# Optimization experiments

Measured on AMD Instinct MI355X. Metric: run time of the kernel, lower is better.

## Reference

```python
import jax, jax.numpy as jnp
import numpy as np

B, S, F = 16, 1024, 768
GRID_SIZE = 5
SPLINE_ORDER = 3
GRID_MIN, GRID_MAX = -1.5, 1.5
EPS = 1e-8  # denominator guard, as in the source


def setup_inputs() -> dict:
    key = jax.random.key(0)
    kx, kc = jax.random.split(key)
    x = jax.random.normal(kx, (B, S, F), dtype=jnp.float32)
    # learned knots: per-feature copy of linspace(grid_range, grid_size)
    knots = jnp.tile(jnp.linspace(GRID_MIN, GRID_MAX, GRID_SIZE, dtype=jnp.float32), (F, 1))  # (F, G)
    coeffs = jax.random.normal(kc, (F, GRID_SIZE + SPLINE_ORDER - 1), dtype=jnp.float32)       # (F, G+k-1)
    scaler = jnp.ones((F,), dtype=jnp.float32)
    return {"x": x, "knots": knots, "coeffs": coeffs, "scaler": scaler}


def _extend_knots(knots, order):
    # pad `order` uniformly-spaced knots on each side: (F, G) -> (F, G + 2*order)
    step = (knots[:, -1] - knots[:, 0]) / (knots.shape[1] - 1)          # (F,)
    left = knots[:, :1] - step[:, None] * jnp.arange(order, 0, -1, dtype=knots.dtype)
    right = knots[:, -1:] + step[:, None] * jnp.arange(1, order + 1, dtype=knots.dtype)
    return jnp.concatenate([left, knots, right], axis=1)


def _bspline_basis(x2d, t_ext, order):
    # x2d: (N, F); t_ext: (F, K). Cox-de Boor, vectorized over basis index.
    t = t_ext[None]          # (1, F, K)
    xe = x2d[..., None]      # (N, F, 1)
    # degree 0: indicator of knot interval -> (N, F, K-1)
    b = ((xe >= t[..., :-1]) & (xe < t[..., 1:])).astype(x2d.dtype)
    for d in range(1, order + 1):
        left = (xe - t[..., :-(d + 1)]) / (t[..., d:-1] - t[..., :-(d + 1)] + EPS) * b[..., :-1]
        right = (t[..., d + 1:] - xe) / (t[..., d + 1:] - t[..., 1:-d] + EPS) * b[..., 1:]
        b = left + right
    return b                 # (N, F, K-1-order)


def reference(x, knots, coeffs, scaler):
    Bsz, Ssz, Feat = x.shape
    x2d = x.reshape(-1, Feat)                       # (N, F)
    t = _extend_knots(knots, SPLINE_ORDER)          # (F, G + 2k)
    basis = _bspline_basis(x2d, t, SPLINE_ORDER)    # (N, F, G+k-1)
    out = jnp.einsum('nfj,fj->nf', basis, coeffs) * scaler
    return out.reshape(Bsz, Ssz, Feat)
```

## Files before the change

### kernel.cpp

```cpp
#include <hip/hip_runtime.h>


constexpr int FEAT  = 768;
constexpr int GSZ   = 5;
constexpr int NCOEF = 7;
constexpr int TPF   = 13;
constexpr int BLK   = 256;
constexpr int NBLK  = 1536;

__global__ __launch_bounds__(256)
void kan_uniform(const float* __restrict__ xg,
                 const float* __restrict__ knots,
                 const float* __restrict__ coeffs,
                 const float* __restrict__ scaler,
                 float* __restrict__ outg,
                 long n2)
{
    __shared__ float clds[2 * TPF * BLK];

    const int  t  = threadIdx.x;
    const long e0 = (long)blockIdx.x * BLK + t;
    const int  f0 = (int)((2 * e0) % FEAT);

    float invh[2], nt0h[2];
#pragma unroll
    for (int c = 0; c < 2; ++c) {
        const int   f  = f0 + c;
        const float k0 = knots[f * GSZ];
        const float k4 = knots[f * GSZ + GSZ - 1];
        const float h  = (k4 - k0) * 0.25f;
        const float iv = 1.0f / h;
        invh[c] = iv;
        nt0h[c] = 3.0f - k0 * iv;
        const float sc = scaler[f];
#pragma unroll
        for (int j = 0; j < 3; ++j) {
            clds[(c * TPF + j) * BLK + t]      = 0.0f;
            clds[(c * TPF + 10 + j) * BLK + t] = 0.0f;
        }
#pragma unroll
        for (int j = 0; j < NCOEF; ++j)
            clds[(c * TPF + 3 + j) * BLK + t] = coeffs[f * NCOEF + j] * sc;
    }
    __syncthreads();

    auto eval = [&](float x, int c) -> float {
        const float g  = fmaf(x, invh[c], nt0h[c]);
        const float fi = floorf(g);
        const int   i  = (int)fi;
        const float w  = g - fi;
        const bool  inr = ((unsigned)i < 10u);
        const int   ic  = min(max(i, 0), 9);
        const float o  = 1.0f - w;
        const float w2 = w * w,  w3 = w2 * w;
        const float o2 = o * o,  o3 = o2 * o;
        const float W0 = o3 * (1.0f / 6.0f);
        const float W3 = w3 * (1.0f / 6.0f);
        const float W1 = fmaf(0.5f, w3, 2.0f / 3.0f) - w2;
        const float W2 = fmaf(0.5f, o3, 2.0f / 3.0f) - o2;
        const float* p = &clds[(c * TPF + ic) * BLK + t];
        float acc =      W0 * p[0];
        acc = fmaf(W1, p[BLK],     acc);
        acc = fmaf(W2, p[2 * BLK], acc);
        acc = fmaf(W3, p[3 * BLK], acc);
        return inr ? acc : 0.0f;
    };

    const float2* __restrict__ xp = (const float2*)xg;
    float2*       __restrict__ op = (float2*)outg;
    const long stride = (long)NBLK * BLK;

    long e = e0;
    for (; e + 3 * stride < n2; e += 4 * stride) {
        const float2 v0 = xp[e];
        const float2 v1 = xp[e + stride];
        const float2 v2 = xp[e + 2 * stride];
        const float2 v3 = xp[e + 3 * stride];
        float2 r0, r1, r2, r3;
        r0.x = eval(v0.x, 0); r0.y = eval(v0.y, 1);
        r1.x = eval(v1.x, 0); r1.y = eval(v1.y, 1);
        r2.x = eval(v2.x, 0); r2.y = eval(v2.y, 1);
        r3.x = eval(v3.x, 0); r3.y = eval(v3.y, 1);
        op[e]              = r0;
        op[e + stride]     = r1;
        op[e + 2 * stride] = r2;
        op[e + 3 * stride] = r3;
    }
    for (; e < n2; e += stride) {
        const float2 v = xp[e];
        float2 r;
        r.x = eval(v.x, 0);
        r.y = eval(v.y, 1);
        op[e] = r;
    }
}

extern "C" void kernel_launch(void* const* d_in, const int* in_sizes, int n_in,
                              void* d_out, int out_size, void* d_ws, size_t ws_size,
                              hipStream_t stream) {
    const float* x      = (const float*)d_in[0];
    const float* knots  = (const float*)d_in[1];
    const float* coeffs = (const float*)d_in[2];
    const float* scaler = (const float*)d_in[3];
    float* out = (float*)d_out;

    const long n2 = (long)in_sizes[0] / 2;

    kan_uniform<<<dim3(NBLK), dim3(BLK), 0, stream>>>(
        x, knots, coeffs, scaler, out, n2);
}
```

Before: 110.9 us.

## Precompute per-feature params in workspace and widen main loop to float4

Adds a small precompute kernel that writes inverse knot spacing, offset, and scaled coefficients to the workspace in a feature-major layout. The main kernel loads these with float4 reads, handles four features per thread with 128-bit loads and stores of x and out, and halves the grid. This cuts the per-block setup and the number of memory instructions. In exchange it adds a second launch and needs twice the LDS per block, which can reduce occupancy.

```diff
diff --git a/kernel.cpp b/kernel.cpp
--- a/kernel.cpp
+++ b/kernel.cpp
@@ -6,42 +6,61 @@
 constexpr int NCOEF = 7;
 constexpr int TPF   = 13;
 constexpr int BLK   = 256;
-constexpr int NBLK  = 1536;
+constexpr int NBLK  = 768;
 
 __global__ __launch_bounds__(256)
-void kan_uniform(const float* __restrict__ xg,
-                 const float* __restrict__ knots,
-                 const float* __restrict__ coeffs,
-                 const float* __restrict__ scaler,
-                 float* __restrict__ outg,
-                 long n2)
+void kan_precompute(const float* __restrict__ knots,
+                    const float* __restrict__ coeffs,
+                    const float* __restrict__ scaler,
+                    float* __restrict__ ws)
 {
-    __shared__ float clds[2 * TPF * BLK];
+    const int f = blockIdx.x * blockDim.x + threadIdx.x;
+    if (f >= FEAT) return;
+    const float k0 = knots[f * GSZ];
+    const float k4 = knots[f * GSZ + GSZ - 1];
+    const float h  = (k4 - k0) * 0.25f;
+    const float iv = 1.0f / h;
+    ws[0 * FEAT + f] = iv;
+    ws[1 * FEAT + f] = 3.0f - k0 * iv;
+    const float sc = scaler[f];
+#pragma unroll
+    for (int j = 0; j < NCOEF; ++j)
+        ws[(2 + j) * FEAT + f] = coeffs[f * NCOEF + j] * sc;
+}
+
+__global__ __launch_bounds__(256)
+void kan_main(const float* __restrict__ xg,
+              const float* __restrict__ ws,
+              float* __restrict__ outg,
+              long n4)
+{
+    __shared__ float clds[4 * TPF * BLK];
 
     const int  t  = threadIdx.x;
     const long e0 = (long)blockIdx.x * BLK + t;
-    const int  f0 = (int)((2 * e0) % FEAT);
+    const int  f0 = (int)((4 * e0) % FEAT);
+    const int  fq = f0 >> 2;
 
-    float invh[2], nt0h[2];
+    const float4* __restrict__ wsv = (const float4*)ws;
+    const float4 ivv = wsv[0 * (FEAT / 4) + fq];
+    const float4 ntv = wsv[1 * (FEAT / 4) + fq];
+    const float invh[4] = {ivv.x, ivv.y, ivv.z, ivv.w};
+    const float nt0h[4] = {ntv.x, ntv.y, ntv.z, ntv.w};
 #pragma unroll
-    for (int c = 0; c < 2; ++c) {
-        const int   f  = f0 + c;
-        const float k0 = knots[f * GSZ];
-        const float k4 = knots[f * GSZ + GSZ - 1];
-        const float h  = (k4 - k0) * 0.25f;
-        const float iv = 1.0f / h;
-        invh[c] = iv;
-        nt0h[c] = 3.0f - k0 * iv;
-        const float sc = scaler[f];
+    for (int j = 0; j < NCOEF; ++j) {
+        const float4 cv = wsv[(2 + j) * (FEAT / 4) + fq];
+        clds[(0 * TPF + 3 + j) * BLK + t] = cv.x;
+        clds[(1 * TPF + 3 + j) * BLK + t] = cv.y;
+        clds[(2 * TPF + 3 + j) * BLK + t] = cv.z;
+        clds[(3 * TPF + 3 + j) * BLK + t] = cv.w;
+    }
+#pragma unroll
+    for (int c = 0; c < 4; ++c)
 #pragma unroll
         for (int j = 0; j < 3; ++j) {
-            clds[(c * TPF + j) * BLK + t]      = 0.0f;
+            clds[(c * TPF + j)      * BLK + t] = 0.0f;
             clds[(c * TPF + 10 + j) * BLK + t] = 0.0f;
         }
-#pragma unroll
-        for (int j = 0; j < NCOEF; ++j)
-            clds[(c * TPF + 3 + j) * BLK + t] = coeffs[f * NCOEF + j] * sc;
-    }
     __syncthreads();
 
     auto eval = [&](float x, int c) -> float {
@@ -66,31 +85,35 @@
         return inr ? acc : 0.0f;
     };
 
-    const float2* __restrict__ xp = (const float2*)xg;
-    float2*       __restrict__ op = (float2*)outg;
+    const float4* __restrict__ xp = (const float4*)xg;
+    float4*       __restrict__ op = (float4*)outg;
     const long stride = (long)NBLK * BLK;
 
     long e = e0;
-    for (; e + 3 * stride < n2; e += 4 * stride) {
-        const float2 v0 = xp[e];
-        const float2 v1 = xp[e + stride];
-        const float2 v2 = xp[e + 2 * stride];
-        const float2 v3 = xp[e + 3 * stride];
-        float2 r0, r1, r2, r3;
+    for (; e + 3 * stride < n4; e += 4 * stride) {
+        const float4 v0 = xp[e];
+        const float4 v1 = xp[e + stride];
+        const float4 v2 = xp[e + 2 * stride];
+        const float4 v3 = xp[e + 3 * stride];
+        float4 r0, r1, r2, r3;
         r0.x = eval(v0.x, 0); r0.y = eval(v0.y, 1);
+        r0.z = eval(v0.z, 2); r0.w = eval(v0.w, 3);
         r1.x = eval(v1.x, 0); r1.y = eval(v1.y, 1);
+        r1.z = eval(v1.z, 2); r1.w = eval(v1.w, 3);
         r2.x = eval(v2.x, 0); r2.y = eval(v2.y, 1);
+        r2.z = eval(v2.z, 2); r2.w = eval(v2.w, 3);
         r3.x = eval(v3.x, 0); r3.y = eval(v3.y, 1);
+        r3.z = eval(v3.z, 2); r3.w = eval(v3.w, 3);
         op[e]              = r0;
         op[e + stride]     = r1;
         op[e + 2 * stride] = r2;
         op[e + 3 * stride] = r3;
     }
-    for (; e < n2; e += stride) {
-        const float2 v = xp[e];
-        float2 r;
-        r.x = eval(v.x, 0);
-        r.y = eval(v.y, 1);
+    for (; e < n4; e += stride) {
+        const float4 v = xp[e];
+        float4 r;
+        r.x = eval(v.x, 0); r.y = eval(v.y, 1);
+        r.z = eval(v.z, 2); r.w = eval(v.w, 3);
         op[e] = r;
     }
 }
@@ -103,9 +126,11 @@
     const float* coeffs = (const float*)d_in[2];
     const float* scaler = (const float*)d_in[3];
     float* out = (float*)d_out;
+    float* ws  = (float*)d_ws;
 
-    const long n2 = (long)in_sizes[0] / 2;
+    const long n4 = (long)in_sizes[0] / 4;
 
-    kan_uniform<<<dim3(NBLK), dim3(BLK), 0, stream>>>(
-        x, knots, coeffs, scaler, out, n2);
+    kan_precompute<<<dim3((FEAT + 255) / 256), dim3(256), 0, stream>>>(
+        knots, coeffs, scaler, ws);
+    kan_main<<<dim3(NBLK), dim3(BLK), 0, stream>>>(x, ws, out, n4);
 }
```

New measurement: 108.6 us. 1.02x faster.
